# Performance work log

Measured on AMD Instinct MI355X. Metric: run time of the kernel, lower is better.

The kernel has to match this reference:

```python
import jax, jax.numpy as jnp
import numpy as np

NEG_SLOPE = 0.2  # PyG GATConv default leaky_relu slope
N_NODES, IN_DIM, HID, HEADS, OUT = 50000, 128, 64, 4, 128
N_EDGES = 800000


def gat_conv(x, src, dst, num_nodes, W, a_src, a_dst, bias, concat):
    """One PyG-style GATConv (add_self_loops already applied to src/dst)."""
    H, C = a_src.shape
    xp = (x @ W).reshape(num_nodes, H, C)            # (N,H,C)
    s = jnp.einsum('nhc,hc->nh', xp, a_src)          # per-node src score
    d = jnp.einsum('nhc,hc->nh', xp, a_dst)          # per-node dst score
    e = s[src] + d[dst]                              # (E,H)
    e = jnp.where(e > 0, e, NEG_SLOPE * e)           # leaky_relu
    # segment softmax over edges grouped by destination node
    m = jax.ops.segment_max(e, dst, num_segments=num_nodes)
    p = jnp.exp(e - m[dst])
    z = jax.ops.segment_sum(p, dst, num_segments=num_nodes)
    alpha = p / (z[dst] + 1e-16)                     # (E,H)
    # scatter-aggregate messages
    out = jax.ops.segment_sum(xp[src] * alpha[:, :, None], dst, num_segments=num_nodes)
    out = out.reshape(num_nodes, H * C) if concat else out.mean(axis=1)
    return out + bias


def setup_inputs() -> dict:
    key = jax.random.key(0)
    ks = jax.random.split(key, 16)
    HC = HEADS * HID
    inp = {
        'x': jax.random.normal(ks[0], (N_NODES, IN_DIM), dtype=jnp.float32),
        'edge_index': jax.random.randint(ks[1], (2, N_EDGES), 0, N_NODES, dtype=jnp.int32),
        'W0': jax.random.normal(ks[2], (IN_DIM, HC), dtype=jnp.float32) * 0.08,
        'a_src0': jax.random.normal(ks[3], (HEADS, HID), dtype=jnp.float32) * 0.1,
        'a_dst0': jax.random.normal(ks[4], (HEADS, HID), dtype=jnp.float32) * 0.1,
        'b0': jnp.zeros((HC,), dtype=jnp.float32),
        'W1': jax.random.normal(ks[5], (HC, HC), dtype=jnp.float32) * 0.06,
        'a_src1': jax.random.normal(ks[6], (HEADS, HID), dtype=jnp.float32) * 0.1,
        'a_dst1': jax.random.normal(ks[7], (HEADS, HID), dtype=jnp.float32) * 0.1,
        'b1': jnp.zeros((HC,), dtype=jnp.float32),
        'W2': jax.random.normal(ks[8], (HC, OUT), dtype=jnp.float32) * 0.06,
        'a_src2': jax.random.normal(ks[9], (1, OUT), dtype=jnp.float32) * 0.1,
        'a_dst2': jax.random.normal(ks[10], (1, OUT), dtype=jnp.float32) * 0.1,
        'b2': jnp.zeros((OUT,), dtype=jnp.float32),
    }
    return inp


def reference(x, edge_index, W0, a_src0, a_dst0, b0, W1, a_src1, a_dst1, b1, W2, a_src2, a_dst2, b2):
    N = x.shape[0]
    loops = jnp.arange(N, dtype=edge_index.dtype)  # add_self_loops=True
    src = jnp.concatenate([edge_index[0], loops])
    dst = jnp.concatenate([edge_index[1], loops])
    h = gat_conv(x, src, dst, N, W0, a_src0, a_dst0, b0, True)
    h = jax.nn.elu(h)
    h = gat_conv(h, src, dst, N, W1, a_src1, a_dst1, b1, True)
    h = jax.nn.elu(h)
    h = gat_conv(h, src, dst, N, W2, a_src2, a_dst2, b2, False)
    return h
```

## Files before the change

### kernel.cpp

```cpp
#include <hip/hip_runtime.h>
#include <hip/hip_bf16.h>
#include <hip/hip_fp16.h>
#include <math.h>

#define N_NODES 50000
#define N_EDGES 800000
#define ET      (N_EDGES + N_NODES)
#define IN_DIM  128
#define HEADS   4
#define HID     64
#define HC      256
#define OUTD    128

typedef _Float16 half8 __attribute__((ext_vector_type(8)));
typedef float f32x4 __attribute__((ext_vector_type(4)));


__global__ void scan1_k(const int* __restrict__ counts, int* __restrict__ offs,
                        int* __restrict__ bsums) {
    __shared__ int sm[512];
    int tid = threadIdx.x;
    int i = blockIdx.x * 512 + tid;
    int v = (i < N_NODES) ? counts[i] : 0;
    sm[tid] = v;
    __syncthreads();
    #pragma unroll
    for (int o = 1; o < 512; o <<= 1) {
        int add = (tid >= o) ? sm[tid - o] : 0;
        __syncthreads();
        sm[tid] += add;
        __syncthreads();
    }
    if (i < N_NODES) offs[i] = sm[tid] - v;
    if (tid == 511) bsums[blockIdx.x] = sm[511];
}

__global__ void scan2_k(int* __restrict__ bsums, int nb) {
    __shared__ int sm[128];
    int tid = threadIdx.x;
    int v = (tid < nb) ? bsums[tid] : 0;
    sm[tid] = v;
    __syncthreads();
    #pragma unroll
    for (int o = 1; o < 128; o <<= 1) {
        int add = (tid >= o) ? sm[tid - o] : 0;
        __syncthreads();
        sm[tid] += add;
        __syncthreads();
    }
    if (tid < nb) bsums[tid] = sm[tid] - v;
}

__global__ void scan3_k(int* __restrict__ offs, const int* __restrict__ bsums) {
    int i = blockIdx.x * 512 + threadIdx.x;
    if (i < N_NODES) offs[i] += bsums[blockIdx.x];
    if (i == 0) offs[N_NODES] = ET;
}

__global__ void fill_k(const int* __restrict__ ei, const int* __restrict__ offs,
                       int* __restrict__ counts, int* __restrict__ csr) {
    int i = blockIdx.x * blockDim.x + threadIdx.x;
    if (i >= ET) return;
    int sv, dv;
    if (i < N_EDGES) { sv = ei[i]; dv = ei[N_EDGES + i]; }
    else             { sv = dv = i - N_EDGES; }
    int pos = offs[dv] + atomicSub(&counts[dv], 1) - 1;
    csr[pos] = sv;
}


#define J_HIST  ET
#define J_CVT   (N_NODES * IN_DIM / 4)
#define J_W     131072
#define SETUP_TOTAL (J_HIST + J_CVT + J_W + 2 * N_NODES)

__global__ void setup_k(const int* __restrict__ ei, int* __restrict__ counts,
                        const float* __restrict__ x, __half* __restrict__ xh,
                        const float* __restrict__ W0, __half* __restrict__ Wt0,
                        const float* __restrict__ W1, __half* __restrict__ Wt1,
                        const float* __restrict__ W2, __half* __restrict__ Wt2,
                        float* __restrict__ S2, float* __restrict__ D2) {
    int g = blockIdx.x * 256 + threadIdx.x;
    if (g < J_HIST) {
        int dv = (g < N_EDGES) ? ei[N_EDGES + g] : (g - N_EDGES);
        atomicAdd(&counts[dv], 1);
        return;
    }
    g -= J_HIST;
    if (g < J_CVT) {
        float4 v = *(const float4*)(x + (size_t)g * 4);
        union { __half2 h2[2]; float2 f2; } u;
        u.h2[0] = __floats2half2_rn(v.x, v.y);
        u.h2[1] = __floats2half2_rn(v.z, v.w);
        *(float2*)(xh + (size_t)g * 4) = u.f2;
        return;
    }
    g -= J_CVT;
    if (g < J_W) {
        if (g < 32768) {
            int n = g / IN_DIM, k = g - n * IN_DIM;
            Wt0[g] = __float2half(W0[(size_t)k * HC + n]);
        } else if (g < 98304) {
            int i = g - 32768;
            int n = i / HC, k = i - n * HC;
            Wt1[i] = __float2half(W1[(size_t)k * HC + n]);
        } else {
            int i = g - 98304;
            int n = i / HC, k = i - n * HC;
            Wt2[i] = __float2half(W2[(size_t)k * OUTD + n]);
        }
        return;
    }
    g -= J_W;
    if (g < N_NODES) { S2[g] = 0.f; return; }
    g -= N_NODES;
    if (g < N_NODES) D2[g] = 0.f;
}


__device__ __forceinline__ void async_copy16(void* lds_base, const void* gaddr) {
    __builtin_amdgcn_global_load_lds(
        (const __attribute__((address_space(1))) unsigned int*)gaddr,
        (__attribute__((address_space(3))) unsigned int*)lds_base,
        16, 0, 0);
}

#define CPAD 132

template<int H, int CD, bool ATOMIC>
__global__ __launch_bounds__(256) void gemm_mfma_k(const __half* __restrict__ A,
                                                   const __half* __restrict__ Wt,
                                                   __half* __restrict__ C,
                                                   const float* __restrict__ asrc,
                                                   const float* __restrict__ adst,
                                                   float* __restrict__ S,
                                                   float* __restrict__ D,
                                                   int M, int K, int N) {
    __shared__ __attribute__((aligned(16))) __half smem[128 * CPAD];
    __half* Ah = smem;
    __half* Bh = smem + 128 * 64;
    const int t = threadIdx.x;
    const int w = t >> 6;
    const int lane = t & 63;
    const int wm = w >> 1, wn = w & 1;
    const int cc = lane & 15;
    const int quad = lane >> 4;
    const int row0 = blockIdx.x * 128;
    const int col0 = blockIdx.y * 128;

    f32x4 acc[4][4];
    #pragma unroll
    for (int i = 0; i < 4; ++i)
        #pragma unroll
        for (int j = 0; j < 4; ++j) acc[i][j] = (f32x4){0.f, 0.f, 0.f, 0.f};

    const int srow = lane >> 3;
    const int skq  = (lane & 7) * 8;

    for (int k0 = 0; k0 < K; k0 += 64) {
        __syncthreads();
        #pragma unroll
        for (int hh = 0; hh < 4; ++hh) {
            int ra = row0 + w * 32 + hh * 8 + srow;
            if (ra > M - 1) ra = M - 1;
            async_copy16(&Ah[(w * 32 + hh * 8) * 64],
                         A + (size_t)ra * K + k0 + skq);
            int rb = col0 + w * 32 + hh * 8 + srow;
            async_copy16(&Bh[(w * 32 + hh * 8) * 64],
                         Wt + (size_t)rb * K + k0 + skq);
        }
        __syncthreads();
        #pragma unroll
        for (int c = 0; c < 2; ++c) {
            half8 a[4], b[4];
            #pragma unroll
            for (int i = 0; i < 4; ++i)
                a[i] = *(const half8*)&Ah[(wm * 64 + i * 16 + cc) * 64 + c * 32 + quad * 8];
            #pragma unroll
            for (int j = 0; j < 4; ++j)
                b[j] = *(const half8*)&Bh[(wn * 64 + j * 16 + cc) * 64 + c * 32 + quad * 8];
            #pragma unroll
            for (int i = 0; i < 4; ++i)
                #pragma unroll
                for (int j = 0; j < 4; ++j)
                    acc[i][j] = __builtin_amdgcn_mfma_f32_16x16x32_f16(b[j], a[i], acc[i][j], 0, 0, 0);
        }
    }

    const int hh_ = ATOMIC ? 0 : (blockIdx.y * 2 + wn);
    float4 asj[4], adj[4];
    #pragma unroll
    for (int j = 0; j < 4; ++j) {
        int cb = (ATOMIC ? wn * 64 : 0) + j * 16 + quad * 4;
        asj[j] = *(const float4*)&asrc[hh_ * CD + cb];
        adj[j] = *(const float4*)&adst[hh_ * CD + cb];
    }
    #pragma unroll
    for (int i = 0; i < 4; ++i) {
        float sv = 0.f, dv = 0.f;
        #pragma unroll
        for (int j = 0; j < 4; ++j) {
            sv = fmaf(acc[i][j][0], asj[j].x, sv); dv = fmaf(acc[i][j][0], adj[j].x, dv);
            sv = fmaf(acc[i][j][1], asj[j].y, sv); dv = fmaf(acc[i][j][1], adj[j].y, dv);
            sv = fmaf(acc[i][j][2], asj[j].z, sv); dv = fmaf(acc[i][j][2], adj[j].z, dv);
            sv = fmaf(acc[i][j][3], asj[j].w, sv); dv = fmaf(acc[i][j][3], adj[j].w, dv);
        }
        sv += __shfl_xor(sv, 16, 64); dv += __shfl_xor(dv, 16, 64);
        sv += __shfl_xor(sv, 32, 64); dv += __shfl_xor(dv, 32, 64);
        int r = row0 + wm * 64 + i * 16 + cc;
        if (quad == 0 && r < M) {
            if constexpr (ATOMIC) {
                atomicAdd(&S[r], sv);
                atomicAdd(&D[r], dv);
            } else {
                S[(size_t)r * H + hh_] = sv;
                D[(size_t)r * H + hh_] = dv;
            }
        }
    }

    __syncthreads();
    #pragma unroll
    for (int i = 0; i < 4; ++i) {
        int tr = wm * 64 + i * 16 + cc;
        #pragma unroll
        for (int j = 0; j < 4; ++j) {
            int tc = wn * 64 + j * 16 + quad * 4;
            union { __half2 h2[2]; uint2 u2; } pk;
            pk.h2[0] = __floats2half2_rn(acc[i][j][0], acc[i][j][1]);
            pk.h2[1] = __floats2half2_rn(acc[i][j][2], acc[i][j][3]);
            *(uint2*)&smem[tr * CPAD + tc] = pk.u2;
        }
    }
    __syncthreads();
    #pragma unroll
    for (int rr = 0; rr < 8; ++rr) {
        int r = rr * 16 + (t >> 4);
        int ccol = (t & 15) * 8;
        uint4 v = *(const uint4*)&smem[r * CPAD + ccol];
        int gr = row0 + r;
        if (gr < M)
            *(uint4*)&C[(size_t)gr * N + col0 + ccol] = v;
    }
}


template<int H, int C, bool ELU_OUT, typename OT>
__global__ __launch_bounds__(256) void aggr_k(const __half* __restrict__ xp,
                                              const float* __restrict__ s,
                                              const float* __restrict__ d,
                                              const int* __restrict__ offs,
                                              const int* __restrict__ csr,
                                              const float* __restrict__ bias,
                                              OT* __restrict__ out) {
    constexpr int HCl = H * C;
    constexpr int EPL = HCl / 64;
    constexpr int U = 8;
    int wid = blockIdx.x * 4 + (threadIdx.x >> 6);
    int lane = threadIdx.x & 63;
    if (wid >= N_NODES) return;
    int h = (lane * EPL) / C;
    float dh = d[(size_t)wid * H + h];
    float z = 0.f;
    float acc[EPL];
    #pragma unroll
    for (int k = 0; k < EPL; ++k) acc[k] = 0.f;

    auto loadrow = [&](int src, float* v) {
        const __half* xr = xp + (size_t)src * HCl + lane * EPL;
        if constexpr (EPL == 4) {
            union { float2 f2; __half2 h2[2]; } u;
            u.f2 = *(const float2*)xr;
            float2 a = __half22float2(u.h2[0]);
            float2 b = __half22float2(u.h2[1]);
            v[0] = a.x; v[1] = a.y; v[2] = b.x; v[3] = b.y;
        } else {
            union { float f; __half2 h2; } u;
            u.f = *(const float*)xr;
            float2 a = __half22float2(u.h2);
            v[0] = a.x; v[1] = a.y;
        }
    };

    int e0 = offs[wid], e1 = offs[wid + 1];
    int j = e0;
    for (; j + U <= e1; j += U) {
        int srcs[U];
        #pragma unroll
        for (int u = 0; u < U; ++u) srcs[u] = csr[j + u];
        float ev[U];
        #pragma unroll
        for (int u = 0; u < U; ++u) ev[u] = s[(size_t)srcs[u] * H + h];
        float v[U][EPL];
        #pragma unroll
        for (int u = 0; u < U; ++u) loadrow(srcs[u], v[u]);
        #pragma unroll
        for (int u = 0; u < U; ++u) {
            float e = ev[u] + dh;
            e = (e > 0.f) ? e : 0.2f * e;
            float p = __expf(e);
            z += p;
            #pragma unroll
            for (int k = 0; k < EPL; ++k) acc[k] += p * v[u][k];
        }
    }
    for (; j < e1; ++j) {
        int sv = csr[j];
        float e = s[(size_t)sv * H + h] + dh;
        e = (e > 0.f) ? e : 0.2f * e;
        float p = __expf(e);
        float v[EPL];
        loadrow(sv, v);
        z += p;
        #pragma unroll
        for (int k = 0; k < EPL; ++k) acc[k] += p * v[k];
    }

    float inv = 1.f / (z + 1e-16f);
    float o[EPL];
    #pragma unroll
    for (int k = 0; k < EPL; ++k) {
        o[k] = acc[k] * inv + bias[lane * EPL + k];
        if constexpr (ELU_OUT) o[k] = (o[k] > 0.f) ? o[k] : (__expf(o[k]) - 1.f);
    }
    if constexpr (sizeof(OT) == 2 && EPL == 4) {
        union { __half2 h2[2]; float2 f2; } u;
        u.h2[0] = __floats2half2_rn(o[0], o[1]);
        u.h2[1] = __floats2half2_rn(o[2], o[3]);
        *(float2*)((__half*)out + (size_t)wid * HCl + lane * EPL) = u.f2;
    } else {
        #pragma unroll
        for (int k = 0; k < EPL; ++k)
            out[(size_t)wid * HCl + lane * EPL + k] = (OT)o[k];
    }
}


extern "C" void kernel_launch(void* const* d_in, const int* in_sizes, int n_in,
                              void* d_out, int out_size, void* d_ws, size_t ws_size,
                              hipStream_t stream) {
    const float* x      = (const float*)d_in[0];
    const int*   ei     = (const int*)  d_in[1];
    const float* W0     = (const float*)d_in[2];
    const float* as0    = (const float*)d_in[3];
    const float* ad0    = (const float*)d_in[4];
    const float* b0     = (const float*)d_in[5];
    const float* W1     = (const float*)d_in[6];
    const float* as1    = (const float*)d_in[7];
    const float* ad1    = (const float*)d_in[8];
    const float* b1     = (const float*)d_in[9];
    const float* W2     = (const float*)d_in[10];
    const float* as2    = (const float*)d_in[11];
    const float* ad2    = (const float*)d_in[12];
    const float* b2     = (const float*)d_in[13];
    float* out = (float*)d_out;

    char* p = (char*)d_ws;
    auto take = [&](size_t bytes) {
        char* r = p;
        p += (bytes + 255) & ~(size_t)255;
        return r;
    };
    __half* XPh   = (__half*)take((size_t)N_NODES * HC * 2);
    __half* Hbuf  = (__half*)take((size_t)N_NODES * HC * 2);
    __half* xh    = (__half*)take((size_t)N_NODES * IN_DIM * 2);
    __half* Wt0   = (__half*)take((size_t)IN_DIM * HC * 2);
    __half* Wt1   = (__half*)take((size_t)HC * HC * 2);
    __half* Wt2   = (__half*)take((size_t)HC * OUTD * 2);
    float*  S     = (float*) take((size_t)N_NODES * HEADS * 4);
    float*  D     = (float*) take((size_t)N_NODES * HEADS * 4);
    float*  S2    = (float*) take((size_t)N_NODES * 4);
    float*  D2    = (float*) take((size_t)N_NODES * 4);
    int*    counts= (int*)   take((size_t)N_NODES * 4);
    int*    offs  = (int*)   take((size_t)(N_NODES + 1) * 4);
    int*    bsums = (int*)   take(512 * 4);
    int*    csr   = (int*)   take((size_t)ET * 4);

    const int NB_SCAN = (N_NODES + 511) / 512;
    const int ET_BLOCKS = (ET + 255) / 256;
    const int NODE_BLOCKS = (N_NODES + 3) / 4;

    hipMemsetAsync(counts, 0, (size_t)N_NODES * 4, stream);
    setup_k<<<(SETUP_TOTAL + 255) / 256, 256, 0, stream>>>(
        ei, counts, x, xh, W0, Wt0, W1, Wt1, W2, Wt2, S2, D2);

    scan1_k<<<NB_SCAN, 512, 0, stream>>>(counts, offs, bsums);
    scan2_k<<<1, 128, 0, stream>>>(bsums, NB_SCAN);
    scan3_k<<<NB_SCAN, 512, 0, stream>>>(offs, bsums);
    fill_k<<<ET_BLOCKS, 256, 0, stream>>>(ei, offs, counts, csr);

    const int MB = (N_NODES + 127) / 128;
    dim3 g0(MB, HC / 128);
    dim3 g2(MB, OUTD / 128);

    gemm_mfma_k<HEADS, HID, false><<<g0, 256, 0, stream>>>(xh, Wt0, XPh, as0, ad0, S, D, N_NODES, IN_DIM, HC);
    aggr_k<HEADS, HID, true, __half><<<NODE_BLOCKS, 256, 0, stream>>>(XPh, S, D, offs, csr, b0, Hbuf);

    gemm_mfma_k<HEADS, HID, false><<<g0, 256, 0, stream>>>(Hbuf, Wt1, XPh, as1, ad1, S, D, N_NODES, HC, HC);
    aggr_k<HEADS, HID, true, __half><<<NODE_BLOCKS, 256, 0, stream>>>(XPh, S, D, offs, csr, b1, Hbuf);

    gemm_mfma_k<1, OUTD, true><<<g2, 256, 0, stream>>>(Hbuf, Wt2, XPh, as2, ad2, S2, D2, N_NODES, HC, OUTD);
    aggr_k<1, OUTD, false, float><<<NODE_BLOCKS, 256, 0, stream>>>(XPh, S2, D2, offs, csr, b2, out);
}
```

Baseline: 412.9 us.

## Store projected features in column-chunked layout and split aggregation across chunks

The GEMM epilogue now writes projected features into 8 column chunks, each holding all nodes contiguously (32 or 16 halves per row), instead of row-major. Aggregation launches 8 blocks per node group, one chunk per block. Each wavefront handles one node and spreads its edges across lane slots, with each lane owning one feature pair, then reduces across slots with shuffles. The goal is a smaller gather working set per chunk for better cache locality, and edge-level parallelism for low-degree nodes. The cost is redundant reads of csr, s and exp per chunk (8x edge-index traffic), plus shuffle reductions.

```diff
diff --git a/kernel.cpp b/kernel.cpp
--- a/kernel.cpp
+++ b/kernel.cpp
@@ -127,7 +127,7 @@
 
 #define CPAD 132
 
-template<int H, int CD, bool ATOMIC>
+template<int H, int CD, bool ATOMIC, int CF>
 __global__ __launch_bounds__(256) void gemm_mfma_k(const __half* __restrict__ A,
                                                    const __half* __restrict__ Wt,
                                                    __half* __restrict__ C,
@@ -237,101 +237,74 @@
     for (int rr = 0; rr < 8; ++rr) {
         int r = rr * 16 + (t >> 4);
         int ccol = (t & 15) * 8;
-        uint4 v = *(const uint4*)&smem[r * CPAD + ccol];
         int gr = row0 + r;
-        if (gr < M)
-            *(uint4*)&C[(size_t)gr * N + col0 + ccol] = v;
-    }
-}
-
-
-template<int H, int C, bool ELU_OUT, typename OT>
-__global__ __launch_bounds__(256) void aggr_k(const __half* __restrict__ xp,
+        if (gr < M) {
+            uint4 v = *(const uint4*)&smem[r * CPAD + ccol];
+            int gc = col0 + ccol;
+            int ch = gc / CF, off = gc % CF;
+            *(uint4*)&C[(size_t)ch * N_NODES * CF + (size_t)gr * CF + off] = v;
+        }
+    }
+}
+
+
+template<int CF, int H, int HCl, bool ELU_OUT, typename OT>
+__global__ __launch_bounds__(256) void aggr_k(const __half* __restrict__ xpc,
                                               const float* __restrict__ s,
                                               const float* __restrict__ d,
                                               const int* __restrict__ offs,
                                               const int* __restrict__ csr,
                                               const float* __restrict__ bias,
                                               OT* __restrict__ out) {
-    constexpr int HCl = H * C;
-    constexpr int EPL = HCl / 64;
-    constexpr int U = 8;
-    int wid = blockIdx.x * 4 + (threadIdx.x >> 6);
-    int lane = threadIdx.x & 63;
+    constexpr int FPAIRS = CF / 2;
+    constexpr int SLOTS  = 64 / FPAIRS;
+    const int chunk = blockIdx.x & 7;
+    const int wid = (blockIdx.x >> 3) * 4 + (threadIdx.x >> 6);
+    const int lane = threadIdx.x & 63;
     if (wid >= N_NODES) return;
-    int h = (lane * EPL) / C;
-    float dh = d[(size_t)wid * H + h];
-    float z = 0.f;
-    float acc[EPL];
-    #pragma unroll
-    for (int k = 0; k < EPL; ++k) acc[k] = 0.f;
-
-    auto loadrow = [&](int src, float* v) {
-        const __half* xr = xp + (size_t)src * HCl + lane * EPL;
-        if constexpr (EPL == 4) {
-            union { float2 f2; __half2 h2[2]; } u;
-            u.f2 = *(const float2*)xr;
-            float2 a = __half22float2(u.h2[0]);
-            float2 b = __half22float2(u.h2[1]);
-            v[0] = a.x; v[1] = a.y; v[2] = b.x; v[3] = b.y;
-        } else {
-            union { float f; __half2 h2; } u;
-            u.f = *(const float*)xr;
-            float2 a = __half22float2(u.h2);
-            v[0] = a.x; v[1] = a.y;
-        }
-    };
-
-    int e0 = offs[wid], e1 = offs[wid + 1];
-    int j = e0;
-    for (; j + U <= e1; j += U) {
-        int srcs[U];
-        #pragma unroll
-        for (int u = 0; u < U; ++u) srcs[u] = csr[j + u];
-        float ev[U];
-        #pragma unroll
-        for (int u = 0; u < U; ++u) ev[u] = s[(size_t)srcs[u] * H + h];
-        float v[U][EPL];
-        #pragma unroll
-        for (int u = 0; u < U; ++u) loadrow(srcs[u], v[u]);
-        #pragma unroll
-        for (int u = 0; u < U; ++u) {
-            float e = ev[u] + dh;
-            e = (e > 0.f) ? e : 0.2f * e;
-            float p = __expf(e);
-            z += p;
-            #pragma unroll
-            for (int k = 0; k < EPL; ++k) acc[k] += p * v[u][k];
-        }
-    }
-    for (; j < e1; ++j) {
-        int sv = csr[j];
-        float e = s[(size_t)sv * H + h] + dh;
+    const int slot = lane / FPAIRS;
+    const int fl   = lane % FPAIRS;
+    const int head = (chunk * CF) / (HCl / H);
+    const __half* xb = xpc + (size_t)chunk * N_NODES * CF + fl * 2;
+    const float dh = d[(size_t)wid * H + head];
+    float z = 0.f, a0 = 0.f, a1 = 0.f;
+
+    const int e0 = offs[wid], e1 = offs[wid + 1];
+    for (int j = e0; j < e1; j += SLOTS) {
+        int idx = j + slot;
+        bool val = idx < e1;
+        int src = csr[val ? idx : e1 - 1];
+        float ev = val ? s[(size_t)src * H + head] : -1e30f;
+        float e = ev + dh;
         e = (e > 0.f) ? e : 0.2f * e;
         float p = __expf(e);
-        float v[EPL];
-        loadrow(sv, v);
-        z += p;
-        #pragma unroll
-        for (int k = 0; k < EPL; ++k) acc[k] += p * v[k];
-    }
-
-    float inv = 1.f / (z + 1e-16f);
-    float o[EPL];
-    #pragma unroll
-    for (int k = 0; k < EPL; ++k) {
-        o[k] = acc[k] * inv + bias[lane * EPL + k];
-        if constexpr (ELU_OUT) o[k] = (o[k] > 0.f) ? o[k] : (__expf(o[k]) - 1.f);
-    }
-    if constexpr (sizeof(OT) == 2 && EPL == 4) {
-        union { __half2 h2[2]; float2 f2; } u;
-        u.h2[0] = __floats2half2_rn(o[0], o[1]);
-        u.h2[1] = __floats2half2_rn(o[2], o[3]);
-        *(float2*)((__half*)out + (size_t)wid * HCl + lane * EPL) = u.f2;
-    } else {
-        #pragma unroll
-        for (int k = 0; k < EPL; ++k)
-            out[(size_t)wid * HCl + lane * EPL + k] = (OT)o[k];
+        union { unsigned r; __half2 h2; } u;
+        u.r = *(const unsigned*)(xb + (size_t)src * CF);
+        float2 v = __half22float2(u.h2);
+        z += p; a0 = fmaf(p, v.x, a0); a1 = fmaf(p, v.y, a1);
+    }
+    #pragma unroll
+    for (int o = FPAIRS; o < 64; o <<= 1) {
+        z  += __shfl_xor(z, o, 64);
+        a0 += __shfl_xor(a0, o, 64);
+        a1 += __shfl_xor(a1, o, 64);
+    }
+    if (slot == 0) {
+        float inv = 1.f / (z + 1e-16f);
+        int fcol = chunk * CF + fl * 2;
+        float o0 = a0 * inv + bias[fcol];
+        float o1 = a1 * inv + bias[fcol + 1];
+        if constexpr (ELU_OUT) {
+            o0 = (o0 > 0.f) ? o0 : (__expf(o0) - 1.f);
+            o1 = (o1 > 0.f) ? o1 : (__expf(o1) - 1.f);
+        }
+        if constexpr (sizeof(OT) == 2) {
+            *(__half2*)((__half*)out + (size_t)wid * HCl + fcol) =
+                __floats2half2_rn(o0, o1);
+        } else {
+            *(float2*)((float*)out + (size_t)wid * HCl + fcol) =
+                make_float2(o0, o1);
+        }
     }
 }
 
@@ -378,7 +351,7 @@
 
     const int NB_SCAN = (N_NODES + 511) / 512;
     const int ET_BLOCKS = (ET + 255) / 256;
-    const int NODE_BLOCKS = (N_NODES + 3) / 4;
+    const int AGGR_BLOCKS = 8 * ((N_NODES + 3) / 4);
 
     hipMemsetAsync(counts, 0, (size_t)N_NODES * 4, stream);
     setup_k<<<(SETUP_TOTAL + 255) / 256, 256, 0, stream>>>(
@@ -393,12 +366,12 @@
     dim3 g0(MB, HC / 128);
     dim3 g2(MB, OUTD / 128);
 
-    gemm_mfma_k<HEADS, HID, false><<<g0, 256, 0, stream>>>(xh, Wt0, XPh, as0, ad0, S, D, N_NODES, IN_DIM, HC);
-    aggr_k<HEADS, HID, true, __half><<<NODE_BLOCKS, 256, 0, stream>>>(XPh, S, D, offs, csr, b0, Hbuf);
-
-    gemm_mfma_k<HEADS, HID, false><<<g0, 256, 0, stream>>>(Hbuf, Wt1, XPh, as1, ad1, S, D, N_NODES, HC, HC);
-    aggr_k<HEADS, HID, true, __half><<<NODE_BLOCKS, 256, 0, stream>>>(XPh, S, D, offs, csr, b1, Hbuf);
-
-    gemm_mfma_k<1, OUTD, true><<<g2, 256, 0, stream>>>(Hbuf, Wt2, XPh, as2, ad2, S2, D2, N_NODES, HC, OUTD);
-    aggr_k<1, OUTD, false, float><<<NODE_BLOCKS, 256, 0, stream>>>(XPh, S2, D2, offs, csr, b2, out);
-}
+    gemm_mfma_k<HEADS, HID, false, 32><<<g0, 256, 0, stream>>>(xh, Wt0, XPh, as0, ad0, S, D, N_NODES, IN_DIM, HC);
+    aggr_k<32, HEADS, HC, true, __half><<<AGGR_BLOCKS, 256, 0, stream>>>(XPh, S, D, offs, csr, b0, Hbuf);
+
+    gemm_mfma_k<HEADS, HID, false, 32><<<g0, 256, 0, stream>>>(Hbuf, Wt1, XPh, as1, ad1, S, D, N_NODES, HC, HC);
+    aggr_k<32, HEADS, HC, true, __half><<<AGGR_BLOCKS, 256, 0, stream>>>(XPh, S, D, offs, csr, b1, Hbuf);
+
+    gemm_mfma_k<1, OUTD, true, 16><<<g2, 256, 0, stream>>>(Hbuf, Wt2, XPh, as2, ad2, S2, D2, N_NODES, HC, OUTD);
+    aggr_k<16, 1, OUTD, false, float><<<AGGR_BLOCKS, 256, 0, stream>>>(XPh, S2, D2, offs, csr, b2, out);
+}
```

After: 782.4 us. +89.5%, slower.

## Compute full 256-wide output per GEMM block to reuse A tile across column halves

Applied to the files above, without the earlier changes.

The GEMM kernel now computes all output column tiles (NH=2 for the 256-wide layers) in one block instead of splitting them across blockIdx.y. The A tile is loaded once per k-step and reused for both weight halves, halving A global reads and block count. In exchange, accumulator registers double (128 floats per thread), which can lower occupancy or cause spills, and there are fewer blocks (391) to spread across the CUs.

```diff
diff --git a/kernel.cpp b/kernel.cpp
--- a/kernel.cpp
+++ b/kernel.cpp
@@ -127,7 +127,7 @@
 
 #define CPAD 132
 
-template<int H, int CD, bool ATOMIC>
+template<int H, int CD, bool ATOMIC, int NH>
 __global__ __launch_bounds__(256) void gemm_mfma_k(const __half* __restrict__ A,
                                                    const __half* __restrict__ Wt,
                                                    __half* __restrict__ C,
@@ -136,9 +136,10 @@
                                                    float* __restrict__ S,
                                                    float* __restrict__ D,
                                                    int M, int K, int N) {
-    __shared__ __attribute__((aligned(16))) __half smem[128 * CPAD];
+    constexpr int SM_HALFS = ((1 + NH) * 128 * 64 > 128 * CPAD)
+                           ? (1 + NH) * 128 * 64 : 128 * CPAD;
+    __shared__ __attribute__((aligned(16))) __half smem[SM_HALFS];
     __half* Ah = smem;
-    __half* Bh = smem + 128 * 64;
     const int t = threadIdx.x;
     const int w = t >> 6;
     const int lane = t & 63;
@@ -146,13 +147,14 @@
     const int cc = lane & 15;
     const int quad = lane >> 4;
     const int row0 = blockIdx.x * 128;
-    const int col0 = blockIdx.y * 128;
-
-    f32x4 acc[4][4];
-    #pragma unroll
-    for (int i = 0; i < 4; ++i)
-        #pragma unroll
-        for (int j = 0; j < 4; ++j) acc[i][j] = (f32x4){0.f, 0.f, 0.f, 0.f};
+
+    f32x4 acc[NH][4][4];
+    #pragma unroll
+    for (int nh = 0; nh < NH; ++nh)
+        #pragma unroll
+        for (int i = 0; i < 4; ++i)
+            #pragma unroll
+            for (int j = 0; j < 4; ++j) acc[nh][i][j] = (f32x4){0.f, 0.f, 0.f, 0.f};
 
     const int srow = lane >> 3;
     const int skq  = (lane & 7) * 8;
@@ -165,82 +167,97 @@
             if (ra > M - 1) ra = M - 1;
             async_copy16(&Ah[(w * 32 + hh * 8) * 64],
                          A + (size_t)ra * K + k0 + skq);
-            int rb = col0 + w * 32 + hh * 8 + srow;
-            async_copy16(&Bh[(w * 32 + hh * 8) * 64],
-                         Wt + (size_t)rb * K + k0 + skq);
+            #pragma unroll
+            for (int nh = 0; nh < NH; ++nh) {
+                int rb = nh * 128 + w * 32 + hh * 8 + srow;
+                async_copy16(&smem[(1 + nh) * 128 * 64 + (w * 32 + hh * 8) * 64],
+                             Wt + (size_t)rb * K + k0 + skq);
+            }
         }
         __syncthreads();
         #pragma unroll
         for (int c = 0; c < 2; ++c) {
-            half8 a[4], b[4];
+            half8 a[4];
             #pragma unroll
             for (int i = 0; i < 4; ++i)
                 a[i] = *(const half8*)&Ah[(wm * 64 + i * 16 + cc) * 64 + c * 32 + quad * 8];
             #pragma unroll
-            for (int j = 0; j < 4; ++j)
-                b[j] = *(const half8*)&Bh[(wn * 64 + j * 16 + cc) * 64 + c * 32 + quad * 8];
-            #pragma unroll
-            for (int i = 0; i < 4; ++i)
+            for (int nh = 0; nh < NH; ++nh) {
+                const __half* Bh = &smem[(1 + nh) * 128 * 64];
+                half8 b[4];
                 #pragma unroll
                 for (int j = 0; j < 4; ++j)
-                    acc[i][j] = __builtin_amdgcn_mfma_f32_16x16x32_f16(b[j], a[i], acc[i][j], 0, 0, 0);
-        }
-    }
-
-    const int hh_ = ATOMIC ? 0 : (blockIdx.y * 2 + wn);
-    float4 asj[4], adj[4];
-    #pragma unroll
-    for (int j = 0; j < 4; ++j) {
-        int cb = (ATOMIC ? wn * 64 : 0) + j * 16 + quad * 4;
-        asj[j] = *(const float4*)&asrc[hh_ * CD + cb];
-        adj[j] = *(const float4*)&adst[hh_ * CD + cb];
-    }
-    #pragma unroll
-    for (int i = 0; i < 4; ++i) {
-        float sv = 0.f, dv = 0.f;
+                    b[j] = *(const half8*)&Bh[(wn * 64 + j * 16 + cc) * 64 + c * 32 + quad * 8];
+                #pragma unroll
+                for (int i = 0; i < 4; ++i)
+                    #pragma unroll
+                    for (int j = 0; j < 4; ++j)
+                        acc[nh][i][j] = __builtin_amdgcn_mfma_f32_16x16x32_f16(b[j], a[i], acc[nh][i][j], 0, 0, 0);
+            }
+        }
+    }
+
+    #pragma unroll
+    for (int nh = 0; nh < NH; ++nh) {
+        const int hh_ = ATOMIC ? 0 : (nh * 2 + wn);
+        float4 asj[4], adj[4];
         #pragma unroll
         for (int j = 0; j < 4; ++j) {
-            sv = fmaf(acc[i][j][0], asj[j].x, sv); dv = fmaf(acc[i][j][0], adj[j].x, dv);
-            sv = fmaf(acc[i][j][1], asj[j].y, sv); dv = fmaf(acc[i][j][1], adj[j].y, dv);
-            sv = fmaf(acc[i][j][2], asj[j].z, sv); dv = fmaf(acc[i][j][2], adj[j].z, dv);
-            sv = fmaf(acc[i][j][3], asj[j].w, sv); dv = fmaf(acc[i][j][3], adj[j].w, dv);
-        }
-        sv += __shfl_xor(sv, 16, 64); dv += __shfl_xor(dv, 16, 64);
-        sv += __shfl_xor(sv, 32, 64); dv += __shfl_xor(dv, 32, 64);
-        int r = row0 + wm * 64 + i * 16 + cc;
-        if (quad == 0 && r < M) {
-            if constexpr (ATOMIC) {
-                atomicAdd(&S[r], sv);
-                atomicAdd(&D[r], dv);
-            } else {
-                S[(size_t)r * H + hh_] = sv;
-                D[(size_t)r * H + hh_] = dv;
-            }
-        }
-    }
-
-    __syncthreads();
-    #pragma unroll
-    for (int i = 0; i < 4; ++i) {
-        int tr = wm * 64 + i * 16 + cc;
-        #pragma unroll
-        for (int j = 0; j < 4; ++j) {
-            int tc = wn * 64 + j * 16 + quad * 4;
-            union { __half2 h2[2]; uint2 u2; } pk;
-            pk.h2[0] = __floats2half2_rn(acc[i][j][0], acc[i][j][1]);
-            pk.h2[1] = __floats2half2_rn(acc[i][j][2], acc[i][j][3]);
-            *(uint2*)&smem[tr * CPAD + tc] = pk.u2;
-        }
-    }
-    __syncthreads();
-    #pragma unroll
-    for (int rr = 0; rr < 8; ++rr) {
-        int r = rr * 16 + (t >> 4);
-        int ccol = (t & 15) * 8;
-        uint4 v = *(const uint4*)&smem[r * CPAD + ccol];
-        int gr = row0 + r;
-        if (gr < M)
-            *(uint4*)&C[(size_t)gr * N + col0 + ccol] = v;
+            int cb = (ATOMIC ? wn * 64 : 0) + j * 16 + quad * 4;
+            asj[j] = *(const float4*)&asrc[hh_ * CD + cb];
+            adj[j] = *(const float4*)&adst[hh_ * CD + cb];
+        }
+        #pragma unroll
+        for (int i = 0; i < 4; ++i) {
+            float sv = 0.f, dv = 0.f;
+            #pragma unroll
+            for (int j = 0; j < 4; ++j) {
+                sv = fmaf(acc[nh][i][j][0], asj[j].x, sv); dv = fmaf(acc[nh][i][j][0], adj[j].x, dv);
+                sv = fmaf(acc[nh][i][j][1], asj[j].y, sv); dv = fmaf(acc[nh][i][j][1], adj[j].y, dv);
+                sv = fmaf(acc[nh][i][j][2], asj[j].z, sv); dv = fmaf(acc[nh][i][j][2], adj[j].z, dv);
+                sv = fmaf(acc[nh][i][j][3], asj[j].w, sv); dv = fmaf(acc[nh][i][j][3], adj[j].w, dv);
+            }
+            sv += __shfl_xor(sv, 16, 64); dv += __shfl_xor(dv, 16, 64);
+            sv += __shfl_xor(sv, 32, 64); dv += __shfl_xor(dv, 32, 64);
+            int r = row0 + wm * 64 + i * 16 + cc;
+            if (quad == 0 && r < M) {
+                if constexpr (ATOMIC) {
+                    atomicAdd(&S[r], sv);
+                    atomicAdd(&D[r], dv);
+                } else {
+                    S[(size_t)r * H + hh_] = sv;
+                    D[(size_t)r * H + hh_] = dv;
+                }
+            }
+        }
+    }
+
+    #pragma unroll
+    for (int nh = 0; nh < NH; ++nh) {
+        __syncthreads();
+        #pragma unroll
+        for (int i = 0; i < 4; ++i) {
+            int tr = wm * 64 + i * 16 + cc;
+            #pragma unroll
+            for (int j = 0; j < 4; ++j) {
+                int tc = wn * 64 + j * 16 + quad * 4;
+                union { __half2 h2[2]; uint2 u2; } pk;
+                pk.h2[0] = __floats2half2_rn(acc[nh][i][j][0], acc[nh][i][j][1]);
+                pk.h2[1] = __floats2half2_rn(acc[nh][i][j][2], acc[nh][i][j][3]);
+                *(uint2*)&smem[tr * CPAD + tc] = pk.u2;
+            }
+        }
+        __syncthreads();
+        #pragma unroll
+        for (int rr = 0; rr < 8; ++rr) {
+            int r = rr * 16 + (t >> 4);
+            int ccol = (t & 15) * 8;
+            int gr = row0 + r;
+            if (gr < M) {
+                uint4 v = *(const uint4*)&smem[r * CPAD + ccol];
+                *(uint4*)&C[(size_t)gr * N + nh * 128 + ccol] = v;
+            }
+        }
     }
 }
 
@@ -379,6 +396,7 @@
     const int NB_SCAN = (N_NODES + 511) / 512;
     const int ET_BLOCKS = (ET + 255) / 256;
     const int NODE_BLOCKS = (N_NODES + 3) / 4;
+    const int MB = (N_NODES + 127) / 128;
 
     hipMemsetAsync(counts, 0, (size_t)N_NODES * 4, stream);
     setup_k<<<(SETUP_TOTAL + 255) / 256, 256, 0, stream>>>(
@@ -389,16 +407,12 @@
     scan3_k<<<NB_SCAN, 512, 0, stream>>>(offs, bsums);
     fill_k<<<ET_BLOCKS, 256, 0, stream>>>(ei, offs, counts, csr);
 
-    const int MB = (N_NODES + 127) / 128;
-    dim3 g0(MB, HC / 128);
-    dim3 g2(MB, OUTD / 128);
-
-    gemm_mfma_k<HEADS, HID, false><<<g0, 256, 0, stream>>>(xh, Wt0, XPh, as0, ad0, S, D, N_NODES, IN_DIM, HC);
+    gemm_mfma_k<HEADS, HID, false, 2><<<MB, 256, 0, stream>>>(xh, Wt0, XPh, as0, ad0, S, D, N_NODES, IN_DIM, HC);
     aggr_k<HEADS, HID, true, __half><<<NODE_BLOCKS, 256, 0, stream>>>(XPh, S, D, offs, csr, b0, Hbuf);
 
-    gemm_mfma_k<HEADS, HID, false><<<g0, 256, 0, stream>>>(Hbuf, Wt1, XPh, as1, ad1, S, D, N_NODES, HC, HC);
+    gemm_mfma_k<HEADS, HID, false, 2><<<MB, 256, 0, stream>>>(Hbuf, Wt1, XPh, as1, ad1, S, D, N_NODES, HC, HC);
     aggr_k<HEADS, HID, true, __half><<<NODE_BLOCKS, 256, 0, stream>>>(XPh, S, D, offs, csr, b1, Hbuf);
 
-    gemm_mfma_k<1, OUTD, true><<<g2, 256, 0, stream>>>(Hbuf, Wt2, XPh, as2, ad2, S2, D2, N_NODES, HC, OUTD);
+    gemm_mfma_k<1, OUTD, true, 1><<<MB, 256, 0, stream>>>(Hbuf, Wt2, XPh, as2, ad2, S2, D2, N_NODES, HC, OUTD);
     aggr_k<1, OUTD, false, float><<<NODE_BLOCKS, 256, 0, stream>>>(XPh, S2, D2, offs, csr, b2, out);
 }
```

Result: slower. 423.7 us (+2.6%).
